# Optimization experiments

Measured on AMD Instinct MI355X. Metric: run time of the kernel, lower is better.

## Reference

```python
import jax, jax.numpy as jnp
import numpy as np

EPS = 1e-9
TEMP = 1.0
TOP_K = 2


def setup_inputs() -> dict:
    key = jax.random.key(0)
    k1, k2, k3, k4 = jax.random.split(key, 4)
    B, T, D, DC, E = 8, 4096, 1024, 512, 64
    din = D + DC
    inputs = jax.random.normal(k1, (B, T, D), dtype=jnp.float32)
    cond = jax.random.normal(k2, (B, T, DC), dtype=jnp.float32)
    # CondRouterMLP params (bias=False): Linear(din -> 2*din), GELU, Linear(2*din -> E)
    W1 = jax.random.normal(k3, (2 * din, din), dtype=jnp.float32) / np.sqrt(din).astype(np.float32)
    W2 = jax.random.normal(k4, (E, 2 * din), dtype=jnp.float32) / np.sqrt(2 * din).astype(np.float32)
    return {"inputs": inputs, "cond": cond, "W1": W1, "W2": W2}


def reference(inputs, cond, W1, W2):
    B, T, D = inputs.shape
    # concat hidden states with condition, flatten tokens
    x = jnp.concatenate([inputs, cond], axis=-1).reshape(-1, D + cond.shape[-1])  # [N, din]
    h = jax.nn.gelu(x @ W1.T, approximate=False)          # [N, 2*din] (torch nn.GELU = exact erf)
    logits = h @ W2.T                                     # [N, E]
    logits = (logits - logits.max(axis=-1, keepdims=True)) / TEMP
    probs = jax.nn.softmax(logits, axis=-1) + EPS
    probs = jnp.clip(probs, EPS, 1.0 - EPS)               # [N, E]
    # eval-mode top-k selection
    top_v, top_i = jax.lax.top_k(probs, TOP_K)            # [N, k]
    N, E = probs.shape
    rows = jnp.arange(N)[:, None]
    router_mask = jnp.zeros_like(probs).at[rows, top_i].set(1.0)
    router_probs = jnp.zeros_like(probs).at[rows, top_i].set(top_v)
    router_probs = router_probs / router_probs.sum(axis=-1, keepdims=True)  # normalize=True
    return (
        router_mask.reshape(B, T, E),
        top_i.reshape(B, T, TOP_K),
        router_probs.reshape(B, T, E),
        probs.reshape(B, T, E),
    )
```

## Files before the change

kernel.cpp:

```cpp
#include <hip/hip_runtime.h>
#include <cmath>

#define N_TOK 32768
#define D0    1024
#define DCC   512
#define DIN   1536
#define JD    3072
#define NE    64
#define BM    128
#define BJ    256
#define BK    32
#define NJC   (JD/BJ)
#define NIT   (DIN/BK)
#define NTH   512
#define HS    36
#define EPSV  1e-9f

typedef _Float16 half8 __attribute__((ext_vector_type(8)));
typedef float    f32x4 __attribute__((ext_vector_type(4)));

#define SZ_A  16384
#define SZ_B  32768
#define OFF_A 0
#define OFF_B 32768
#define LDS_TOTAL 98304
#define OFF_H    0
#define OFF_LRED 0
#define OFF_EPI  36864

#define W1T_G (192*3072)
#define W2T_G (384*64)

__device__ __forceinline__ f32x4 mfma16(half8 a, half8 b, f32x4 c) {
    return __builtin_amdgcn_mfma_f32_16x16x32_f16(a, b, c, 0, 0, 0);
}

__device__ __forceinline__ void split8(const float4 v0, const float4 v1, half8& hh, half8& hl) {
    float f[8] = {v0.x, v0.y, v0.z, v0.w, v1.x, v1.y, v1.z, v1.w};
    #pragma unroll
    for (int i = 0; i < 8; ++i) {
        _Float16 h = (_Float16)f[i];
        hh[i] = h;
        hl[i] = (_Float16)(f[i] - (float)h);
    }
}

__device__ __forceinline__ void gload16(const void* g, void* l) {
    __builtin_amdgcn_global_load_lds(
        (const __attribute__((address_space(1))) unsigned int*)g,
        (__attribute__((address_space(3))) unsigned int*)l, 16, 0, 0);
}

__global__ void presplit_w1t(const float* __restrict__ W1,
                             _Float16* __restrict__ hi, _Float16* __restrict__ lo) {
    int g = blockIdx.x * blockDim.x + threadIdx.x;
    if (g >= W1T_G) return;
    const int j  = g % JD;
    const int ko = g / JD;
    const float* src = W1 + (size_t)j * DIN + ko * 8;
    float4 v0 = *(const float4*)src;
    float4 v1 = *(const float4*)(src + 4);
    half8 h, l;
    split8(v0, v1, h, l);
    *(half8*)(hi + (size_t)g * 8) = h;
    *(half8*)(lo + (size_t)g * 8) = l;
}

__global__ void presplit_w2t(const float* __restrict__ W2,
                             _Float16* __restrict__ hi, _Float16* __restrict__ lo) {
    int g = blockIdx.x * blockDim.x + threadIdx.x;
    if (g >= W2T_G) return;
    const int e  = g & 63;
    const int jo = g >> 6;
    const float* src = W2 + (size_t)e * JD + jo * 8;
    float4 v0 = *(const float4*)src;
    float4 v1 = *(const float4*)(src + 4);
    half8 h, l;
    split8(v0, v1, h, l);
    *(half8*)(hi + (size_t)g * 8) = h;
    *(half8*)(lo + (size_t)g * 8) = l;
}

__global__ __launch_bounds__(NTH, 1)
void router_v9(const float* __restrict__ inp, const float* __restrict__ cnd,
               const _Float16* __restrict__ W1h, const _Float16* __restrict__ W1l,
               const _Float16* __restrict__ W2h, const _Float16* __restrict__ W2l,
               float* __restrict__ out_mask, float* __restrict__ out_topi,
               float* __restrict__ out_rp, float* __restrict__ out_probs)
{
    __shared__ __align__(16) char smem[LDS_TOTAL];

    const int tid  = threadIdx.x;
    const int lane = tid & 63;
    const int w    = tid >> 6;
    const int tg   = w >> 2;
    const int jg   = w & 3;
    const int l15  = lane & 15;
    const int lg   = lane >> 4;
    const int t0   = blockIdx.x * BM;

    const int akoct = w >> 1;
    const int arow  = (w & 1) * 64 + lane;
    const int bplane = w >> 2;
    const int bkoct  = w & 3;

    int aoff[4], boff[4];
    #pragma unroll
    for (int tf = 0; tf < 4; ++tf) aoff[tf] = (lg*128 + tg*64 + tf*16 + l15) * 16;
    #pragma unroll
    for (int jf = 0; jf < 4; ++jf) boff[jf] = (lg*256 + jg*64 + jf*16 + l15) * 16;

    const f32x4 vzero = {0.f, 0.f, 0.f, 0.f};
    f32x4 lacc[4] = {vzero, vzero, vzero, vzero};

    const float* const xrowA = inp + (size_t)(t0 + arow) * D0;
    const float* const xrowC = cnd + (size_t)(t0 + arow) * DCC;
    const _Float16* const Wbp = bplane ? W1l : W1h;

    _Float16* const myHh = (_Float16*)(smem + OFF_H + w * 9216);
    _Float16* const myHl = myHh + 2304;

    for (int jc = 0; jc < NJC; ++jc) {
        f32x4 acc1[4][4];
        #pragma unroll
        for (int tf = 0; tf < 4; ++tf)
            #pragma unroll
            for (int jf = 0; jf < 4; ++jf) acc1[tf][jf] = vzero;

        {
            #pragma unroll
            for (int q = 0; q < 4; ++q) {
                const _Float16* src = Wbp + ((size_t)bkoct * JD + jc*BJ + q*64 + lane) * 8;
                char* dst = smem + OFF_B + bplane*16384 + bkoct*4096 + q*1024;
                gload16(src, dst);
            }
            const float* sx = xrowA + akoct * 8;
            float4 v0 = *(const float4*)sx;
            float4 v1 = *(const float4*)(sx + 4);
            half8 hh, hl;
            split8(v0, v1, hh, hl);
            const int g = (akoct*128 + arow) * 16;
            *(half8*)(smem + OFF_A + g) = hh;
            *(half8*)(smem + OFF_A + 8192 + g) = hl;
        }
        __syncthreads();

        for (int it = 0; it < NIT; ++it) {
            const int cur = it & 1, nxt = cur ^ 1;
            const bool more = (it + 1 < NIT);
            float4 xv0, xv1;
            if (more) {
                const int ko = (it + 1) * 4 + bkoct;
                #pragma unroll
                for (int q = 0; q < 4; ++q) {
                    const _Float16* src = Wbp + ((size_t)ko * JD + jc*BJ + q*64 + lane) * 8;
                    char* dst = smem + OFF_B + nxt*SZ_B + bplane*16384 + bkoct*4096 + q*1024;
                    gload16(src, dst);
                }
                const int k = (it + 1) * BK + akoct * 8;
                const float* sx = (k < D0) ? (xrowA + k) : (xrowC + k - D0);
                xv0 = *(const float4*)sx;
                xv1 = *(const float4*)(sx + 4);
            }
            const char* ab = smem + OFF_A + cur*SZ_A;
            const char* bb = smem + OFF_B + cur*SZ_B;
            half8 ah[4], al[4], bh[4], bl[4];
            #pragma unroll
            for (int tf = 0; tf < 4; ++tf) {
                ah[tf] = *(const half8*)(ab + aoff[tf]);
                al[tf] = *(const half8*)(ab + 8192 + aoff[tf]);
            }
            #pragma unroll
            for (int jf = 0; jf < 4; ++jf) {
                bh[jf] = *(const half8*)(bb + boff[jf]);
                bl[jf] = *(const half8*)(bb + 16384 + boff[jf]);
            }
            #pragma unroll
            for (int tf = 0; tf < 4; ++tf)
                #pragma unroll
                for (int jf = 0; jf < 4; ++jf) {
                    acc1[tf][jf] = mfma16(ah[tf], bh[jf], acc1[tf][jf]);
                    acc1[tf][jf] = mfma16(ah[tf], bl[jf], acc1[tf][jf]);
                    acc1[tf][jf] = mfma16(al[tf], bh[jf], acc1[tf][jf]);
                }
            if (more) {
                half8 hh, hl;
                split8(xv0, xv1, hh, hl);
                const int g = (akoct*128 + arow) * 16;
                *(half8*)(smem + OFF_A + nxt*SZ_A + g) = hh;
                *(half8*)(smem + OFF_A + nxt*SZ_A + 8192 + g) = hl;
            }
            __syncthreads();
        }

        #pragma unroll
        for (int r = 0; r < 2; ++r) {
            #pragma unroll
            for (int c = 0; c < 2; ++c) {
                const int jf = 2*r + c;
                #pragma unroll
                for (int tf = 0; tf < 4; ++tf)
                    #pragma unroll
                    for (int rr = 0; rr < 4; ++rr) {
                        const float v = acc1[tf][jf][rr];
                        const float gv = 0.5f * v * (1.0f + erff(v * 0.70710678118654752f));
                        const _Float16 gh = (_Float16)gv;
                        const _Float16 gl = (_Float16)(gv - (float)gh);
                        const int o = (tf*16 + lg*4 + rr) * HS + c*16 + l15;
                        myHh[o] = gh; myHl[o] = gl;
                    }
            }
            __syncthreads();
            #pragma unroll
            for (int s = 0; s < 4; ++s) {
                const _Float16* sh = (const _Float16*)(smem + OFF_H + (tg*4 + s) * 9216);
                const _Float16* sl = sh + 2304;
                const int jo = jc*32 + s*8 + r*4 + lg;
                const size_t wg = ((size_t)jo * 64 + jg*16 + l15) * 8;
                half8 b2h = *(const half8*)(W2h + wg);
                half8 b2l = *(const half8*)(W2l + wg);
                #pragma unroll
                for (int tf = 0; tf < 4; ++tf) {
                    const int o = (tf*16 + l15) * HS + lg*8;
                    half8 a2h = *(const half8*)(sh + o);
                    half8 a2l = *(const half8*)(sl + o);
                    lacc[tf] = mfma16(a2h, b2h, lacc[tf]);
                    lacc[tf] = mfma16(a2h, b2l, lacc[tf]);
                    lacc[tf] = mfma16(a2l, b2h, lacc[tf]);
                }
            }
            __syncthreads();
        }
    }

    float* const Lred = (float*)(smem + OFF_LRED);
    #pragma unroll
    for (int tf = 0; tf < 4; ++tf)
        #pragma unroll
        for (int rr = 0; rr < 4; ++rr)
            Lred[(tg*64 + tf*16 + lg*4 + rr) * 68 + jg*16 + l15] = lacc[tf][rr];
    __syncthreads();

    float* const mA   = (float*)(smem + OFF_EPI);
    float* const invA = mA + BM;
    int*   const i1A  = (int*)(invA + BM);
    int*   const i2A  = i1A + BM;
    float* const rp1A = (float*)(i2A + BM);
    float* const rp2A = rp1A + BM;

    if (tid < BM) {
        const float* row = Lred + tid * 68;
        float m = -3.402823466e38f;
        for (int e = 0; e < NE; ++e) m = fmaxf(m, row[e]);
        float s = 0.f, v1 = -3.402823466e38f, v2 = -3.402823466e38f;
        int i1 = 0, i2 = 0;
        for (int e = 0; e < NE; ++e) {
            const float v = row[e];
            s += expf(v - m);
            if (v > v1)      { v2 = v1; i2 = i1; v1 = v; i1 = e; }
            else if (v > v2) { v2 = v; i2 = e; }
        }
        const float inv = 1.f / s;
        const float p1 = fminf(expf(v1 - m) * inv + EPSV, 1.f - EPSV);
        const float p2 = fminf(expf(v2 - m) * inv + EPSV, 1.f - EPSV);
        mA[tid] = m; invA[tid] = inv; i1A[tid] = i1; i2A[tid] = i2;
        const float den = p1 + p2;
        rp1A[tid] = p1 / den; rp2A[tid] = p2 / den;
    }
    __syncthreads();

    for (int idx = tid; idx < BM * NE; idx += NTH) {
        const int r = idx >> 6, e = idx & 63;
        const size_t o = (size_t)(t0 + r) * NE + e;
        const float p = fminf(expf(Lred[r * 68 + e] - mA[r]) * invA[r] + EPSV, 1.f - EPSV);
        const int b1 = (e == i1A[r]), b2 = (e == i2A[r]);
        out_probs[o] = p;
        out_mask[o]  = (b1 | b2) ? 1.f : 0.f;
        out_rp[o]    = b1 ? rp1A[r] : (b2 ? rp2A[r] : 0.f);
    }
    if (tid < BM * 2) {
        const int r = tid >> 1, q = tid & 1;
        out_topi[(size_t)(t0 + r) * 2 + q] = (float)(q ? i2A[r] : i1A[r]);
    }
}

extern "C" void kernel_launch(void* const* d_in, const int* in_sizes, int n_in,
                              void* d_out, int out_size, void* d_ws, size_t ws_size,
                              hipStream_t stream) {
    const float* inp = (const float*)d_in[0];
    const float* cnd = (const float*)d_in[1];
    const float* W1  = (const float*)d_in[2];
    const float* W2  = (const float*)d_in[3];

    float* out = (float*)d_out;
    const size_t NT = (size_t)N_TOK;
    float* out_mask  = out;
    float* out_topi  = out + NT * NE;
    float* out_rp    = out + NT * NE + NT * 2;
    float* out_probs = out + NT * NE + NT * 2 + NT * NE;

    _Float16* W1h = (_Float16*)d_ws;
    _Float16* W1l = W1h + (size_t)W1T_G * 8;
    _Float16* W2h = W1l + (size_t)W1T_G * 8;
    _Float16* W2l = W2h + (size_t)W2T_G * 8;

    hipLaunchKernelGGL(presplit_w1t, dim3((W1T_G + 255) / 256), dim3(256), 0, stream, W1, W1h, W1l);
    hipLaunchKernelGGL(presplit_w2t, dim3((W2T_G + 255) / 256), dim3(256), 0, stream, W2, W2h, W2l);
    hipLaunchKernelGGL(router_v9, dim3(N_TOK / BM), dim3(NTH), 0, stream,
                       inp, cnd, W1h, W1l, W2h, W2l,
                       out_mask, out_topi, out_rp, out_probs);
}
```

Baseline: 1.098 ms.

## Pre-split activations to fp16 hi/lo and load GEMM fragments directly from global

Adds a pre-pass that converts the concatenated input and condition tensors into fp16 hi/lo planes in workspace. The main kernel then drops LDS staging for the first GEMM and loads MFMA fragments straight from global memory, with a two-stage register double buffer and no per-iteration barriers. The aim is to remove LDS traffic, barrier stalls and the repeated in-kernel splitting of activations. In exchange it writes and re-reads a large workspace copy of X and relies on uncoalesced per-lane global loads. The old kernel remains as a fallback when the workspace is too small.

```diff
diff --git a/kernel.cpp b/kernel.cpp
--- a/kernel.cpp
+++ b/kernel.cpp
@@ -9,9 +9,8 @@
 #define NE    64
 #define BM    128
 #define BJ    256
-#define BK    32
 #define NJC   (JD/BJ)
-#define NIT   (DIN/BK)
+#define NIT   48
 #define NTH   512
 #define HS    36
 #define EPSV  1e-9f
@@ -19,17 +18,16 @@
 typedef _Float16 half8 __attribute__((ext_vector_type(8)));
 typedef float    f32x4 __attribute__((ext_vector_type(4)));
 
-#define SZ_A  16384
-#define SZ_B  32768
-#define OFF_A 0
-#define OFF_B 32768
-#define LDS_TOTAL 98304
-#define OFF_H    0
-#define OFF_LRED 0
-#define OFF_EPI  36864
-
+#define W1N   ((size_t)JD*DIN)
+#define W2N   ((size_t)NE*JD)
+#define XTN   ((size_t)N_TOK*DIN)
+#define XTG   (N_TOK*192)
 #define W1T_G (192*3072)
 #define W2T_G (384*64)
+
+#define V15_LDS   73728
+#define V15_LRED  0
+#define V15_EPI   36864
 
 __device__ __forceinline__ f32x4 mfma16(half8 a, half8 b, f32x4 c) {
     return __builtin_amdgcn_mfma_f32_16x16x32_f16(a, b, c, 0, 0, 0);
@@ -81,14 +79,56 @@
     *(half8*)(lo + (size_t)g * 8) = l;
 }
 
+__global__ void presplit_x(const float* __restrict__ inp, const float* __restrict__ cnd,
+                           _Float16* __restrict__ hi, _Float16* __restrict__ lo) {
+    int g = blockIdx.x * blockDim.x + threadIdx.x;
+    if (g >= XTG) return;
+    const int token = g / 192;
+    const int ko    = g % 192;
+    const float* src = (ko < 128) ? (inp + (size_t)token * D0 + ko * 8)
+                                  : (cnd + (size_t)token * DCC + (ko - 128) * 8);
+    float4 v0 = *(const float4*)src;
+    float4 v1 = *(const float4*)(src + 4);
+    half8 h, l;
+    split8(v0, v1, h, l);
+    *(half8*)(hi + (size_t)g * 8) = h;
+    *(half8*)(lo + (size_t)g * 8) = l;
+}
+
+#define LOAD_FRAGS(AH, AL, BH, BL, IT) do {                                   \
+    _Pragma("unroll")                                                         \
+    for (int tf_ = 0; tf_ < 4; ++tf_) {                                       \
+        const _Float16* p_ = baseX[tf_] + (size_t)(IT) * 32;                  \
+        AH[tf_] = *(const half8*)p_;                                          \
+        AL[tf_] = *(const half8*)(p_ + XTN);                                  \
+    }                                                                         \
+    _Pragma("unroll")                                                         \
+    for (int jf_ = 0; jf_ < 4; ++jf_) {                                       \
+        const _Float16* p_ = baseW[jf_] + (size_t)(IT) * 98304;               \
+        BH[jf_] = *(const half8*)p_;                                          \
+        BL[jf_] = *(const half8*)(p_ + W1N);                                  \
+    }                                                                         \
+} while (0)
+
+#define DO_MFMA(AH, AL, BH, BL) do {                                          \
+    _Pragma("unroll")                                                         \
+    for (int tf_ = 0; tf_ < 4; ++tf_)                                         \
+        _Pragma("unroll")                                                     \
+        for (int jf_ = 0; jf_ < 4; ++jf_) {                                   \
+            acc1[tf_][jf_] = mfma16(AH[tf_], BH[jf_], acc1[tf_][jf_]);        \
+            acc1[tf_][jf_] = mfma16(AH[tf_], BL[jf_], acc1[tf_][jf_]);        \
+            acc1[tf_][jf_] = mfma16(AL[tf_], BH[jf_], acc1[tf_][jf_]);        \
+        }                                                                     \
+} while (0)
+
 __global__ __launch_bounds__(NTH, 1)
-void router_v9(const float* __restrict__ inp, const float* __restrict__ cnd,
-               const _Float16* __restrict__ W1h, const _Float16* __restrict__ W1l,
-               const _Float16* __restrict__ W2h, const _Float16* __restrict__ W2l,
-               float* __restrict__ out_mask, float* __restrict__ out_topi,
-               float* __restrict__ out_rp, float* __restrict__ out_probs)
+void router_v15(const _Float16* __restrict__ Xh,
+                const _Float16* __restrict__ W1h,
+                const _Float16* __restrict__ W2h, const _Float16* __restrict__ W2l,
+                float* __restrict__ out_mask, float* __restrict__ out_topi,
+                float* __restrict__ out_rp, float* __restrict__ out_probs)
 {
-    __shared__ __align__(16) char smem[LDS_TOTAL];
+    __shared__ __align__(16) char smem[V15_LDS];
 
     const int tid  = threadIdx.x;
     const int lane = tid & 63;
@@ -99,25 +139,15 @@
     const int lg   = lane >> 4;
     const int t0   = blockIdx.x * BM;
 
-    const int akoct = w >> 1;
-    const int arow  = (w & 1) * 64 + lane;
-    const int bplane = w >> 2;
-    const int bkoct  = w & 3;
-
-    int aoff[4], boff[4];
+    const _Float16* baseX[4];
     #pragma unroll
-    for (int tf = 0; tf < 4; ++tf) aoff[tf] = (lg*128 + tg*64 + tf*16 + l15) * 16;
-    #pragma unroll
-    for (int jf = 0; jf < 4; ++jf) boff[jf] = (lg*256 + jg*64 + jf*16 + l15) * 16;
+    for (int tf = 0; tf < 4; ++tf)
+        baseX[tf] = Xh + (size_t)(t0 + tg*64 + tf*16 + l15) * DIN + lg*8;
 
     const f32x4 vzero = {0.f, 0.f, 0.f, 0.f};
     f32x4 lacc[4] = {vzero, vzero, vzero, vzero};
 
-    const float* const xrowA = inp + (size_t)(t0 + arow) * D0;
-    const float* const xrowC = cnd + (size_t)(t0 + arow) * DCC;
-    const _Float16* const Wbp = bplane ? W1l : W1h;
-
-    _Float16* const myHh = (_Float16*)(smem + OFF_H + w * 9216);
+    _Float16* const myHh = (_Float16*)(smem + w * 9216);
     _Float16* const myHl = myHh + 2304;
 
     for (int jc = 0; jc < NJC; ++jc) {
@@ -127,70 +157,19 @@
             #pragma unroll
             for (int jf = 0; jf < 4; ++jf) acc1[tf][jf] = vzero;
 
-        {
-            #pragma unroll
-            for (int q = 0; q < 4; ++q) {
-                const _Float16* src = Wbp + ((size_t)bkoct * JD + jc*BJ + q*64 + lane) * 8;
-                char* dst = smem + OFF_B + bplane*16384 + bkoct*4096 + q*1024;
-                gload16(src, dst);
-            }
-            const float* sx = xrowA + akoct * 8;
-            float4 v0 = *(const float4*)sx;
-            float4 v1 = *(const float4*)(sx + 4);
-            half8 hh, hl;
-            split8(v0, v1, hh, hl);
-            const int g = (akoct*128 + arow) * 16;
-            *(half8*)(smem + OFF_A + g) = hh;
-            *(half8*)(smem + OFF_A + 8192 + g) = hl;
-        }
-        __syncthreads();
-
-        for (int it = 0; it < NIT; ++it) {
-            const int cur = it & 1, nxt = cur ^ 1;
-            const bool more = (it + 1 < NIT);
-            float4 xv0, xv1;
-            if (more) {
-                const int ko = (it + 1) * 4 + bkoct;
-                #pragma unroll
-                for (int q = 0; q < 4; ++q) {
-                    const _Float16* src = Wbp + ((size_t)ko * JD + jc*BJ + q*64 + lane) * 8;
-                    char* dst = smem + OFF_B + nxt*SZ_B + bplane*16384 + bkoct*4096 + q*1024;
-                    gload16(src, dst);
-                }
-                const int k = (it + 1) * BK + akoct * 8;
-                const float* sx = (k < D0) ? (xrowA + k) : (xrowC + k - D0);
-                xv0 = *(const float4*)sx;
-                xv1 = *(const float4*)(sx + 4);
-            }
-            const char* ab = smem + OFF_A + cur*SZ_A;
-            const char* bb = smem + OFF_B + cur*SZ_B;
-            half8 ah[4], al[4], bh[4], bl[4];
-            #pragma unroll
-            for (int tf = 0; tf < 4; ++tf) {
-                ah[tf] = *(const half8*)(ab + aoff[tf]);
-                al[tf] = *(const half8*)(ab + 8192 + aoff[tf]);
-            }
-            #pragma unroll
-            for (int jf = 0; jf < 4; ++jf) {
-                bh[jf] = *(const half8*)(bb + boff[jf]);
-                bl[jf] = *(const half8*)(bb + 16384 + boff[jf]);
-            }
-            #pragma unroll
-            for (int tf = 0; tf < 4; ++tf)
-                #pragma unroll
-                for (int jf = 0; jf < 4; ++jf) {
-                    acc1[tf][jf] = mfma16(ah[tf], bh[jf], acc1[tf][jf]);
-                    acc1[tf][jf] = mfma16(ah[tf], bl[jf], acc1[tf][jf]);
-                    acc1[tf][jf] = mfma16(al[tf], bh[jf], acc1[tf][jf]);
-                }
-            if (more) {
-                half8 hh, hl;
-                split8(xv0, xv1, hh, hl);
-                const int g = (akoct*128 + arow) * 16;
-                *(half8*)(smem + OFF_A + nxt*SZ_A + g) = hh;
-                *(half8*)(smem + OFF_A + nxt*SZ_A + 8192 + g) = hl;
-            }
-            __syncthreads();
+        const _Float16* baseW[4];
+        #pragma unroll
+        for (int jf = 0; jf < 4; ++jf)
+            baseW[jf] = W1h + ((size_t)lg*3072 + jc*BJ + jg*64 + jf*16 + l15) * 8;
+
+        half8 a0h[4], a0l[4], b0h[4], b0l[4];
+        half8 a1h[4], a1l[4], b1h[4], b1l[4];
+        LOAD_FRAGS(a0h, a0l, b0h, b0l, 0);
+        for (int it = 0; it < NIT; it += 2) {
+            if (it + 1 < NIT) LOAD_FRAGS(a1h, a1l, b1h, b1l, it + 1);
+            DO_MFMA(a0h, a0l, b0h, b0l);
+            if (it + 2 < NIT) LOAD_FRAGS(a0h, a0l, b0h, b0l, it + 2);
+            if (it + 1 < NIT) DO_MFMA(a1h, a1l, b1h, b1l);
         }
 
         #pragma unroll
@@ -213,7 +192,7 @@
             __syncthreads();
             #pragma unroll
             for (int s = 0; s < 4; ++s) {
-                const _Float16* sh = (const _Float16*)(smem + OFF_H + (tg*4 + s) * 9216);
+                const _Float16* sh = (const _Float16*)(smem + (tg*4 + s) * 9216);
                 const _Float16* sl = sh + 2304;
                 const int jo = jc*32 + s*8 + r*4 + lg;
                 const size_t wg = ((size_t)jo * 64 + jg*16 + l15) * 8;
@@ -233,7 +212,7 @@
         }
     }
 
-    float* const Lred = (float*)(smem + OFF_LRED);
+    float* const Lred = (float*)(smem + V15_LRED);
     #pragma unroll
     for (int tf = 0; tf < 4; ++tf)
         #pragma unroll
@@ -241,7 +220,7 @@
             Lred[(tg*64 + tf*16 + lg*4 + rr) * 68 + jg*16 + l15] = lacc[tf][rr];
     __syncthreads();
 
-    float* const mA   = (float*)(smem + OFF_EPI);
+    float* const mA   = (float*)(smem + V15_EPI);
     float* const invA = mA + BM;
     int*   const i1A  = (int*)(invA + BM);
     int*   const i2A  = i1A + BM;
@@ -284,6 +263,205 @@
     }
 }
 
+#define V9_SZ_A  16384
+#define V9_SZ_B  32768
+#define V9_OFF_B 32768
+#define V9_LDS   98304
+#define V9_LRED  0
+#define V9_EPI   36864
+
+__global__ __launch_bounds__(NTH, 1)
+void router_v9fb(const float* __restrict__ inp, const float* __restrict__ cnd,
+                 const _Float16* __restrict__ W1h, const _Float16* __restrict__ W1l,
+                 const _Float16* __restrict__ W2h, const _Float16* __restrict__ W2l,
+                 float* __restrict__ out_mask, float* __restrict__ out_topi,
+                 float* __restrict__ out_rp, float* __restrict__ out_probs)
+{
+    __shared__ __align__(16) char smem[V9_LDS];
+    const int tid  = threadIdx.x;
+    const int lane = tid & 63;
+    const int w    = tid >> 6;
+    const int tg   = w >> 2;
+    const int jg   = w & 3;
+    const int l15  = lane & 15;
+    const int lg   = lane >> 4;
+    const int t0   = blockIdx.x * BM;
+    const int akoct = w >> 1;
+    const int arow  = (w & 1) * 64 + lane;
+    const int bplane = w >> 2;
+    const int bkoct  = w & 3;
+
+    int aoff[4], boff[4];
+    #pragma unroll
+    for (int tf = 0; tf < 4; ++tf) aoff[tf] = (lg*128 + tg*64 + tf*16 + l15) * 16;
+    #pragma unroll
+    for (int jf = 0; jf < 4; ++jf) boff[jf] = (lg*256 + jg*64 + jf*16 + l15) * 16;
+
+    const f32x4 vzero = {0.f, 0.f, 0.f, 0.f};
+    f32x4 lacc[4] = {vzero, vzero, vzero, vzero};
+    const float* const xrowA = inp + (size_t)(t0 + arow) * D0;
+    const float* const xrowC = cnd + (size_t)(t0 + arow) * DCC;
+    const _Float16* const Wbp = bplane ? W1l : W1h;
+    _Float16* const myHh = (_Float16*)(smem + w * 9216);
+    _Float16* const myHl = myHh + 2304;
+
+    for (int jc = 0; jc < NJC; ++jc) {
+        f32x4 acc1[4][4];
+        #pragma unroll
+        for (int tf = 0; tf < 4; ++tf)
+            #pragma unroll
+            for (int jf = 0; jf < 4; ++jf) acc1[tf][jf] = vzero;
+        {
+            #pragma unroll
+            for (int q = 0; q < 4; ++q) {
+                const _Float16* src = Wbp + ((size_t)bkoct * JD + jc*BJ + q*64 + lane) * 8;
+                char* dst = smem + V9_OFF_B + bplane*16384 + bkoct*4096 + q*1024;
+                gload16(src, dst);
+            }
+            const float* sx = xrowA + akoct * 8;
+            float4 v0 = *(const float4*)sx;
+            float4 v1 = *(const float4*)(sx + 4);
+            half8 hh, hl;
+            split8(v0, v1, hh, hl);
+            const int g = (akoct*128 + arow) * 16;
+            *(half8*)(smem + g) = hh;
+            *(half8*)(smem + 8192 + g) = hl;
+        }
+        __syncthreads();
+        for (int it = 0; it < NIT; ++it) {
+            const int cur = it & 1, nxt = cur ^ 1;
+            const bool more = (it + 1 < NIT);
+            float4 xv0, xv1;
+            if (more) {
+                const int ko = (it + 1) * 4 + bkoct;
+                #pragma unroll
+                for (int q = 0; q < 4; ++q) {
+                    const _Float16* src = Wbp + ((size_t)ko * JD + jc*BJ + q*64 + lane) * 8;
+                    char* dst = smem + V9_OFF_B + nxt*V9_SZ_B + bplane*16384 + bkoct*4096 + q*1024;
+                    gload16(src, dst);
+                }
+                const int k = (it + 1) * 32 + akoct * 8;
+                const float* sx = (k < D0) ? (xrowA + k) : (xrowC + k - D0);
+                xv0 = *(const float4*)sx;
+                xv1 = *(const float4*)(sx + 4);
+            }
+            const char* ab = smem + cur*V9_SZ_A;
+            const char* bb = smem + V9_OFF_B + cur*V9_SZ_B;
+            half8 ah[4], al[4], bh[4], bl[4];
+            #pragma unroll
+            for (int tf = 0; tf < 4; ++tf) {
+                ah[tf] = *(const half8*)(ab + aoff[tf]);
+                al[tf] = *(const half8*)(ab + 8192 + aoff[tf]);
+            }
+            #pragma unroll
+            for (int jf = 0; jf < 4; ++jf) {
+                bh[jf] = *(const half8*)(bb + boff[jf]);
+                bl[jf] = *(const half8*)(bb + 16384 + boff[jf]);
+            }
+            #pragma unroll
+            for (int tf = 0; tf < 4; ++tf)
+                #pragma unroll
+                for (int jf = 0; jf < 4; ++jf) {
+                    acc1[tf][jf] = mfma16(ah[tf], bh[jf], acc1[tf][jf]);
+                    acc1[tf][jf] = mfma16(ah[tf], bl[jf], acc1[tf][jf]);
+                    acc1[tf][jf] = mfma16(al[tf], bh[jf], acc1[tf][jf]);
+                }
+            if (more) {
+                half8 hh, hl;
+                split8(xv0, xv1, hh, hl);
+                const int g = (akoct*128 + arow) * 16;
+                *(half8*)(smem + nxt*V9_SZ_A + g) = hh;
+                *(half8*)(smem + nxt*V9_SZ_A + 8192 + g) = hl;
+            }
+            __syncthreads();
+        }
+        #pragma unroll
+        for (int r = 0; r < 2; ++r) {
+            #pragma unroll
+            for (int c = 0; c < 2; ++c) {
+                const int jf = 2*r + c;
+                #pragma unroll
+                for (int tf = 0; tf < 4; ++tf)
+                    #pragma unroll
+                    for (int rr = 0; rr < 4; ++rr) {
+                        const float v = acc1[tf][jf][rr];
+                        const float gv = 0.5f * v * (1.0f + erff(v * 0.70710678118654752f));
+                        const _Float16 gh = (_Float16)gv;
+                        const _Float16 gl = (_Float16)(gv - (float)gh);
+                        const int o = (tf*16 + lg*4 + rr) * HS + c*16 + l15;
+                        myHh[o] = gh; myHl[o] = gl;
+                    }
+            }
+            __syncthreads();
+            #pragma unroll
+            for (int s = 0; s < 4; ++s) {
+                const _Float16* sh = (const _Float16*)(smem + (tg*4 + s) * 9216);
+                const _Float16* sl = sh + 2304;
+                const int jo = jc*32 + s*8 + r*4 + lg;
+                const size_t wg = ((size_t)jo * 64 + jg*16 + l15) * 8;
+                half8 b2h = *(const half8*)(W2h + wg);
+                half8 b2l = *(const half8*)(W2l + wg);
+                #pragma unroll
+                for (int tf = 0; tf < 4; ++tf) {
+                    const int o = (tf*16 + l15) * HS + lg*8;
+                    half8 a2h = *(const half8*)(sh + o);
+                    half8 a2l = *(const half8*)(sl + o);
+                    lacc[tf] = mfma16(a2h, b2h, lacc[tf]);
+                    lacc[tf] = mfma16(a2h, b2l, lacc[tf]);
+                    lacc[tf] = mfma16(a2l, b2h, lacc[tf]);
+                }
+            }
+            __syncthreads();
+        }
+    }
+    float* const Lred = (float*)(smem + V9_LRED);
+    #pragma unroll
+    for (int tf = 0; tf < 4; ++tf)
+        #pragma unroll
+        for (int rr = 0; rr < 4; ++rr)
+            Lred[(tg*64 + tf*16 + lg*4 + rr) * 68 + jg*16 + l15] = lacc[tf][rr];
+    __syncthreads();
+    float* const mA   = (float*)(smem + V9_EPI);
+    float* const invA = mA + BM;
+    int*   const i1A  = (int*)(invA + BM);
+    int*   const i2A  = i1A + BM;
+    float* const rp1A = (float*)(i2A + BM);
+    float* const rp2A = rp1A + BM;
+    if (tid < BM) {
+        const float* row = Lred + tid * 68;
+        float m = -3.402823466e38f;
+        for (int e = 0; e < NE; ++e) m = fmaxf(m, row[e]);
+        float s = 0.f, v1 = -3.402823466e38f, v2 = -3.402823466e38f;
+        int i1 = 0, i2 = 0;
+        for (int e = 0; e < NE; ++e) {
+            const float v = row[e];
+            s += expf(v - m);
+            if (v > v1)      { v2 = v1; i2 = i1; v1 = v; i1 = e; }
+            else if (v > v2) { v2 = v; i2 = e; }
+        }
+        const float inv = 1.f / s;
+        const float p1 = fminf(expf(v1 - m) * inv + EPSV, 1.f - EPSV);
+        const float p2 = fminf(expf(v2 - m) * inv + EPSV, 1.f - EPSV);
+        mA[tid] = m; invA[tid] = inv; i1A[tid] = i1; i2A[tid] = i2;
+        const float den = p1 + p2;
+        rp1A[tid] = p1 / den; rp2A[tid] = p2 / den;
+    }
+    __syncthreads();
+    for (int idx = tid; idx < BM * NE; idx += NTH) {
+        const int r = idx >> 6, e = idx & 63;
+        const size_t o = (size_t)(t0 + r) * NE + e;
+        const float p = fminf(expf(Lred[r * 68 + e] - mA[r]) * invA[r] + EPSV, 1.f - EPSV);
+        const int b1 = (e == i1A[r]), b2 = (e == i2A[r]);
+        out_probs[o] = p;
+        out_mask[o]  = (b1 | b2) ? 1.f : 0.f;
+        out_rp[o]    = b1 ? rp1A[r] : (b2 ? rp2A[r] : 0.f);
+    }
+    if (tid < BM * 2) {
+        const int r = tid >> 1, q = tid & 1;
+        out_topi[(size_t)(t0 + r) * 2 + q] = (float)(q ? i2A[r] : i1A[r]);
+    }
+}
+
 extern "C" void kernel_launch(void* const* d_in, const int* in_sizes, int n_in,
                               void* d_out, int out_size, void* d_ws, size_t ws_size,
                               hipStream_t stream) {
@@ -299,14 +477,28 @@
     float* out_rp    = out + NT * NE + NT * 2;
     float* out_probs = out + NT * NE + NT * 2 + NT * NE;
 
-    _Float16* W1h = (_Float16*)d_ws;
-    _Float16* W1l = W1h + (size_t)W1T_G * 8;
-    _Float16* W2h = W1l + (size_t)W1T_G * 8;
-    _Float16* W2l = W2h + (size_t)W2T_G * 8;
-
-    hipLaunchKernelGGL(presplit_w1t, dim3((W1T_G + 255) / 256), dim3(256), 0, stream, W1, W1h, W1l);
-    hipLaunchKernelGGL(presplit_w2t, dim3((W2T_G + 255) / 256), dim3(256), 0, stream, W2, W2h, W2l);
-    hipLaunchKernelGGL(router_v9, dim3(N_TOK / BM), dim3(NTH), 0, stream,
-                       inp, cnd, W1h, W1l, W2h, W2l,
-                       out_mask, out_topi, out_rp, out_probs);
-}
+    const size_t V15_REQ = (2*XTN + 2*W1N + 2*W2N) * 2;
+    if (ws_size >= V15_REQ) {
+        _Float16* Xh  = (_Float16*)d_ws;
+        _Float16* Xl  = Xh + XTN;
+        _Float16* W1h = Xl + XTN;
+        _Float16* W1l = W1h + W1N;
+        _Float16* W2h = W1l + W1N;
+        _Float16* W2l = W2h + W2N;
+        hipLaunchKernelGGL(presplit_x,   dim3(XTG/256), dim3(256), 0, stream, inp, cnd, Xh, Xl);
+        hipLaunchKernelGGL(presplit_w1t, dim3((W1T_G + 255)/256), dim3(256), 0, stream, W1, W1h, W1l);
+        hipLaunchKernelGGL(presplit_w2t, dim3((W2T_G + 255)/256), dim3(256), 0, stream, W2, W2h, W2l);
+        hipLaunchKernelGGL(router_v15, dim3(N_TOK / BM), dim3(NTH), 0, stream,
+                           Xh, W1h, W2h, W2l, out_mask, out_topi, out_rp, out_probs);
+    } else {
+        _Float16* W1h = (_Float16*)d_ws;
+        _Float16* W1l = W1h + W1N;
+        _Float16* W2h = W1l + W1N;
+        _Float16* W2l = W2h + W2N;
+        hipLaunchKernelGGL(presplit_w1t, dim3((W1T_G + 255)/256), dim3(256), 0, stream, W1, W1h, W1l);
+        hipLaunchKernelGGL(presplit_w2t, dim3((W2T_G + 255)/256), dim3(256), 0, stream, W2, W2h, W2l);
+        hipLaunchKernelGGL(router_v9fb, dim3(N_TOK / BM), dim3(NTH), 0, stream,
+                           inp, cnd, W1h, W1l, W2h, W2l,
+                           out_mask, out_topi, out_rp, out_probs);
+    }
+}
```

Measured after the change: 1.659 ms. +51.2%, slower.
